# Optimization experiments

Measured on AMD Instinct MI355X. Metric: run time of the kernel, lower is better.

Reference implementation:

```python
import jax, jax.numpy as jnp
import numpy as np

# ---- static configuration (matches init_kwargs / input_specs) ----
B, T, C = 32, 4096, 3
SCALES = 128
KLF = 10                      # kernel_length_factor
OUT_H, OUT_W = 224, 224
PRECISION = 12
N_PSI = 2 ** PRECISION        # 4096 samples of the integrated wavelet
XMIN, XMAX = -8.0, 8.0        # pywt 'mexh' support
SPAN = XMAX - XMIN
STEP = SPAN / (N_PSI - 1)     # x_master[1] - x_master[0]
MAX_SCALE = T // (2 * KLF)
SCALES_VEC = np.logspace(np.log10(2.0), np.log10(MAX_SCALE), SCALES).astype(np.float32)

# Per-scale gather indices (static: derived from constant scales_vec / x_master grid)
# j = floor(arange(scale*span + 1) / (scale*step)), clipped to valid range.
J_LIST = []
for s in SCALES_VEC:
    s = float(s)
    n = int(np.ceil(s * SPAN + 1.0))
    j = np.floor(np.arange(n, dtype=np.float64) / (s * STEP)).astype(np.int32)
    J_LIST.append(np.clip(j, 0, N_PSI - 1))


def _mexh_int_psi():
    """Integrated Mexican-hat wavelet, exactly as pywt wavefun + CWTLayer build()."""
    x = np.linspace(XMIN, XMAX, N_PSI)
    psi = (2.0 / (np.sqrt(3.0) * np.pi ** 0.25)) * (1.0 - x ** 2) * np.exp(-x ** 2 / 2.0)
    dt = x[1] - x[0]
    int_psi = np.cumsum(psi) * dt
    int_psi -= np.mean(int_psi)
    int_psi /= np.sqrt(np.sum(np.abs(int_psi) ** 2))
    return int_psi.astype(np.float32)


def setup_inputs() -> dict:
    key = jax.random.key(0)
    x = jax.random.normal(key, (B, T, C), dtype=jnp.float32)
    int_psi_base = jnp.asarray(_mexh_int_psi())
    return {"x": x, "int_psi_base": int_psi_base}


def reference(x, int_psi_base):
    pad = min((N_PSI - 1) // 2, T - 1)                       # 2047
    xp = jnp.pad(x, ((0, 0), (pad, pad), (0, 0)), mode="reflect")
    xp = jnp.transpose(xp, (2, 0, 1)).reshape(C * B, T + 2 * pad, 1)  # NWC

    coefs = []
    for s, j in zip(SCALES_VEC, J_LIST):
        # dynamic-length wavelet kernel built by gather, flipped (as in the layer)
        kern = jnp.flip(jnp.take(int_psi_base, jnp.asarray(j), axis=0))[:, None, None]  # (K,1,1) WIO
        conv = jax.lax.conv_general_dilated(
            xp, kern, window_strides=(1,), padding="VALID",
            dimension_numbers=("NWC", "WIO", "NWC"))[..., 0]  # (CB, Lc)
        coef = -jnp.sqrt(jnp.float32(s)) * (conv[:, 1:] - conv[:, :-1])
        d = max((coef.shape[-1] - T) // 2, 0)
        coefs.append(jax.lax.dynamic_slice_in_dim(coef, d, T, axis=1))

    out = jnp.stack(coefs, axis=1)                    # (C*B, SCALES, T)
    out = out.reshape(C, B, SCALES, T).transpose(1, 2, 3, 0)  # (B, SCALES, T, C)
    out = jax.image.resize(out, (B, OUT_H, OUT_W, C), method="bilinear")
    return out
```

## Files before the change

### kernel.cpp

```cpp
#include <hip/hip_runtime.h>
#include <cmath>
#include <cstdint>


constexpr int C_TP     = 8190;
constexpr int C_XROWS  = 8192;
constexpr long long C_HSTRIDE = 3776;
constexpr int C_HGUARD = 160;
constexpr int C_NCLS   = 9;
constexpr int C_RW     = 8;
constexpr int C_NCH    = 28;
constexpr int C_NW     = 224;
constexpr int C_SIGP   = 128;
constexpr int C_M      = 512;
constexpr int C_NP     = 7;
constexpr int C_SQ     = 64;

typedef float v2f __attribute__((ext_vector_type(2)));
typedef float v4f __attribute__((ext_vector_type(4)));

__device__ __forceinline__ void scale_params(int i, float& s32, int& K, int& d, double& a) {
  const double l2   = log10(2.0);
  const double l204 = log10(204.0);
  double step = (l204 - l2) / 127.0;
  double e = (i == 127) ? l204 : ((double)i * step + l2);
  double sv = pow(10.0, e);
  s32 = (float)sv;
  double sp = (double)s32;
  K = (int)ceil(sp * 16.0 + 1.0);
  d = (4094 - K) >> 1;
  a = sp * (16.0 / 4095.0);
}

__global__ __launch_bounds__(256) void k_build_H(const float* __restrict__ int_psi,
                                                 const float* __restrict__ x,
                                                 float* __restrict__ Hbuf,
                                                 int* __restrict__ meta,
                                                 float* __restrict__ xpQ,
                                                 float* __restrict__ OT) {
  int i   = blockIdx.x;
  int cls = blockIdx.y;

  if (cls == 9) {
    float4* otz = (float4*)OT + (long long)i * 7168;
    float4 z4 = make_float4(0.f, 0.f, 0.f, 0.f);
    for (int q = threadIdx.x; q < 7168; q += 256) otz[q] = z4;
    for (int q = threadIdx.x; q < 8192; q += 256) {
      int idx = i * 8192 + q;
      int r   = idx & 127;
      int p   = idx >> 7;
      int g   = r >> 2;
      int e   = r & 3;
      float val = 0.f;
      if (e < 3 && p < C_TP) {
        int t = p - 2047;
        if (t < 0) t = -t;
        else if (t > 4095) t = 8190 - t;
        val = x[(g * 4096 + t) * 3 + e];
      }
      xpQ[idx] = val;
    }
    return;
  }

  float s32; int K, d; double a;
  scale_params(i, s32, K, d, a);

  int wr = (cls < 7) ? ((cls == 0) ? 7 : cls) : ((cls == 7) ? 0 : 223);
  double ks = 4096.0 / 224.0;
  double sf = ((double)wr + 0.5) * ks - 0.5;
  int t_lo = (int)floor(sf - ks) + 1;
  int t_hi = (int)ceil(sf + ks) - 1;
  if (t_lo < 0) t_lo = 0;
  if (t_hi > 4095) t_hi = 4095;
  int nt  = t_hi - t_lo + 1;
  int npv = nt + 1;

  int p_lo = t_lo + d;
  int Lh   = K + npv - 1;
  int kr   = (cls == 0) ? 1 : ((cls == 8) ? 31 : 0);
  int off0 = p_lo - 128 * kr;
  int shift = off0 & 3;
  int offA  = off0 - shift;
  int rowLen = (shift + Lh + 3) & ~3;

  __shared__ double Wt_sh[40];
  __shared__ float  v_shf[40];
  __shared__ float  kern_sh[3352];

  float* rowFull = Hbuf + (long long)(i * C_NCLS + cls) * C_HSTRIDE;
  int g0 = C_HGUARD + shift;
  int g1 = g0 + Lh;
  for (int q = threadIdx.x; q < g0; q += 256) rowFull[q] = 0.f;
  for (int q = g1 + threadIdx.x; q < (int)C_HSTRIDE; q += 256) rowFull[q] = 0.f;

  if (threadIdx.x == 0) {
    double Z = 0.0;
    for (int t = 0; t < nt; ++t) {
      double wv = 1.0 - fabs(sf - (double)(t + t_lo)) / ks;
      if (wv < 0.0) wv = 0.0;
      Wt_sh[t] = wv; Z += wv;
    }
    for (int t = 0; t < nt; ++t) Wt_sh[t] = Wt_sh[t] / Z;
    double sq = sqrt((double)s32);
    for (int q = 0; q < 40; ++q) {
      double wm1 = (q >= 1 && q <= nt)  ? Wt_sh[q - 1] : 0.0;
      double w0  = (q < nt)             ? Wt_sh[q]     : 0.0;
      v_shf[q] = (float)(-sq * (wm1 - w0));
    }
  }

  float* kernp = kern_sh + 40;
  int fillN = K + 80;
  for (int q = threadIdx.x; q < fillN; q += 256) {
    int tau = q - 40;
    float kv = 0.f;
    if (tau >= 0 && tau < K) {
      int u = K - 1 - tau;
      int jj = (int)floor((double)u / a);
      jj = jj < 0 ? 0 : (jj > 4095 ? 4095 : jj);
      kv = int_psi[jj];
    }
    kern_sh[q] = kv;
  }
  __syncthreads();

  float* row = rowFull + C_HGUARD;
  for (int q = threadIdx.x; q < Lh; q += 256) {
    float acc = 0.f;
    for (int t = 0; t < npv; ++t) acc += v_shf[t] * kernp[q - t];
    row[shift + q] = acc;
  }
  if (threadIdx.x == 0) {
    meta[(i * C_NCLS + cls) * 2 + 0] = offA;
    meta[(i * C_NCLS + cls) * 2 + 1] = rowLen;
  }
}

__global__ __launch_bounds__(64, 4) void k_cwt_main(const float* __restrict__ xpQ,
                                                    const float* __restrict__ Hbuf,
                                                    const int* __restrict__ meta,
                                                    float* __restrict__ OT) {
  int piece = blockIdx.x;
  int chunk = blockIdx.y;
  int i     = 127 - blockIdx.z;
  int lane  = threadIdx.x;
  int g     = lane & 31;
  int half  = lane >> 5;

  __shared__ v4f Hs[C_RW][C_SQ];

  v2f accL[C_RW], accH[C_RW];
  const float* rowP[C_RW];
  int startj[C_RW];
  int U0 = 0x7fffffff, U1 = 0;
#pragma unroll
  for (int j = 0; j < C_RW; ++j) {
    accL[j] = (v2f){0.f, 0.f};
    accH[j] = (v2f){0.f, 0.f};
    int w = chunk * C_RW + j;
    int cls = (w == 0) ? 7 : ((w == 223) ? 8 : (w % 7));
    int k = w / 7;
    int base = i * C_NCLS + cls;
    int offA = meta[base * 2 + 0];
    int rl   = meta[base * 2 + 1];
    int start = offA + 128 * k;
    startj[j] = start;
    if (start < U0) U0 = start;
    if (start + rl > U1) U1 = start + rl;
    rowP[j] = Hbuf + (long long)base * C_HSTRIDE;
  }

  int m0 = U0 + piece * C_M;
  int m1 = m0 + C_M; if (m1 > U1) m1 = U1;
  if (m0 >= m1) return;

  int len = m1 - m0;
  int nIt = (len + 7) >> 3;

  for (int ph = 0; ph < 2; ++ph) {
    int it0 = ph << 5;
    if (it0 >= nIt) break;
    int it1 = nIt < it0 + 32 ? nIt : it0 + 32;
    int qn  = 2 * (it1 - it0);

#pragma unroll
    for (int j = 0; j < C_RW; ++j) {
      const float* src = rowP[j] + (C_HGUARD + m0 - startj[j]) + 8 * it0;
      if (lane < qn) Hs[j][lane] = *(const v4f*)(src + 4 * lane);
    }
    __syncthreads();

    const float* xr = xpQ + ((long long)(m0 + 8 * it0 + 4 * half) << 7) + (g << 2);
#pragma unroll 2
    for (int it = it0; it < it1; ++it) {
      v4f xv0 = *(const v4f*)(xr);
      v4f xv1 = *(const v4f*)(xr + 128);
      v4f xv2 = *(const v4f*)(xr + 256);
      v4f xv3 = *(const v4f*)(xr + 384);
      xr += 1024;
      int lq = 2 * (it - it0) + half;
#pragma unroll
      for (int j = 0; j < C_RW; ++j) {
        v4f h = Hs[j][lq];
        accL[j] += xv0.xy * h.x; accH[j] += xv0.zw * h.x;
        accL[j] += xv1.xy * h.y; accH[j] += xv1.zw * h.y;
        accL[j] += xv2.xy * h.z; accH[j] += xv2.zw * h.z;
        accL[j] += xv3.xy * h.w; accH[j] += xv3.zw * h.w;
      }
    }
    __syncthreads();
  }

#pragma unroll
  for (int j = 0; j < C_RW; ++j) {
    float s0 = accL[j].x, s1 = accL[j].y, s2 = accH[j].x, s3 = accH[j].y;
    s0 += __shfl_xor(s0, 32);
    s1 += __shfl_xor(s1, 32);
    s2 += __shfl_xor(s2, 32);
    s3 += __shfl_xor(s3, 32);
    if (lane < 32) {
      int w = chunk * C_RW + j;
      float* dst = OT + ((long long)i * C_NW + w) * C_SIGP;
      atomicAdd(dst + g,      s0);
      atomicAdd(dst + 32 + g, s1);
      atomicAdd(dst + 64 + g, s2);
      atomicAdd(dst + 96 + g, s3);
    }
  }
}

__global__ __launch_bounds__(256) void k_final(const float* __restrict__ OT,
                                               float* __restrict__ out) {
  int wt = blockIdx.x;
  int h  = blockIdx.y;

  float inv = 128.0f / 224.0f;
  float sg = ((float)h + 0.5f) * inv - 0.5f;
  float sgf = floorf(sg);
  int s0 = (int)sgf;
  float fr = sg - sgf;
  int r0, r1;
  if (s0 < 0)        { r0 = 0;   r1 = 0;   fr = 0.f; }
  else if (s0 >= 127){ r0 = 127; r1 = 127; fr = 0.f; }
  else               { r0 = s0;  r1 = s0 + 1; }

  __shared__ float sh0[8 * 132];
  __shared__ float sh1[8 * 132];
  for (int q = threadIdx.x; q < 1024; q += 256) {
    int wp  = q >> 7;
    int sg2 = q & 127;
    int wg  = wt * 8 + wp;
    sh0[wp * 132 + sg2] = OT[((long long)r0 * C_NW + wg) * C_SIGP + sg2];
    sh1[wp * 132 + sg2] = OT[((long long)r1 * C_NW + wg) * C_SIGP + sg2];
  }
  __syncthreads();

  int b  = threadIdx.x >> 3;
  int wp = threadIdx.x & 7;
  int obase = ((b * 224 + h) * 224 + wt * 8 + wp) * 3;
#pragma unroll
  for (int c = 0; c < 3; ++c) {
    int sidx = wp * 132 + c * 32 + b;
    float a0 = sh0[sidx];
    float a1 = sh1[sidx];
    out[obase + c] = (1.0f - fr) * a0 + fr * a1;
  }
}

extern "C" void kernel_launch(void* const* d_in, const int* in_sizes, int n_in,
                              void* d_out, int out_size, void* d_ws, size_t ws_size,
                              hipStream_t stream) {
  const float* x       = (const float*)d_in[0];
  const float* int_psi = (const float*)d_in[1];
  float* out = (float*)d_out;

  float* xpQ  = (float*)d_ws;
  float* Hbuf = xpQ + (long long)C_XROWS * C_SIGP;
  int*   meta = (int*)(Hbuf + (long long)128 * C_NCLS * C_HSTRIDE);
  float* OT   = (float*)(meta + 2304);

  k_build_H<<<dim3(128, 10), dim3(256), 0, stream>>>(int_psi, x, Hbuf, meta, xpQ, OT);
  k_cwt_main<<<dim3(C_NP, C_NCH, 128), dim3(64), 0, stream>>>(xpQ, Hbuf, meta, OT);
  k_final<<<dim3(28, 224), dim3(256), 0, stream>>>(OT, out);
}
```

Before: 204.1 us.

## Widen CWT register tile to 16 output columns and prefetch signal rows

Each CWT block now accumulates 16 output columns instead of 8, so every loaded signal vector is reused across twice as many filter rows. The number of column chunks is halved and the shared filter staging is split into four 16-iteration phases with 32-entry buffers. The signal loads are software-pipelined one iteration ahead. Filter row pointers are recomputed during staging instead of held in registers, and the H buffer gets a zeroed front pad and a larger stride to cover out-of-range reads. The wider tile doubles accumulator registers, which may lower occupancy, and the prefetch reads one row group past the end.

Result: slower. 412.2 us (+102.0%).

```diff
diff --git a/kernel.cpp b/kernel.cpp
--- a/kernel.cpp
+++ b/kernel.cpp
@@ -5,16 +5,17 @@
 
 constexpr int C_TP     = 8190;
 constexpr int C_XROWS  = 8192;
-constexpr long long C_HSTRIDE = 3776;
+constexpr long long C_HSTRIDE = 3968;
 constexpr int C_HGUARD = 160;
+constexpr int C_HPAD   = 512;
 constexpr int C_NCLS   = 9;
-constexpr int C_RW     = 8;
-constexpr int C_NCH    = 28;
+constexpr int C_RW     = 16;
+constexpr int C_NCH    = 14;
 constexpr int C_NW     = 224;
 constexpr int C_SIGP   = 128;
 constexpr int C_M      = 512;
-constexpr int C_NP     = 7;
-constexpr int C_SQ     = 64;
+constexpr int C_NP     = 8;
+constexpr int C_SQ     = 32;
 
 typedef float v2f __attribute__((ext_vector_type(2)));
 typedef float v4f __attribute__((ext_vector_type(4)));
@@ -45,6 +46,10 @@
     float4* otz = (float4*)OT + (long long)i * 7168;
     float4 z4 = make_float4(0.f, 0.f, 0.f, 0.f);
     for (int q = threadIdx.x; q < 7168; q += 256) otz[q] = z4;
+    if (i == 0) {
+      float* pad = Hbuf - C_HPAD;
+      for (int q = threadIdx.x; q < C_HPAD; q += 256) pad[q] = 0.f;
+    }
     for (int q = threadIdx.x; q < 8192; q += 256) {
       int idx = i * 8192 + q;
       int r   = idx & 127;
@@ -151,8 +156,6 @@
   __shared__ v4f Hs[C_RW][C_SQ];
 
   v2f accL[C_RW], accH[C_RW];
-  const float* rowP[C_RW];
-  int startj[C_RW];
   int U0 = 0x7fffffff, U1 = 0;
 #pragma unroll
   for (int j = 0; j < C_RW; ++j) {
@@ -160,54 +163,67 @@
     accH[j] = (v2f){0.f, 0.f};
     int w = chunk * C_RW + j;
     int cls = (w == 0) ? 7 : ((w == 223) ? 8 : (w % 7));
-    int k = w / 7;
     int base = i * C_NCLS + cls;
     int offA = meta[base * 2 + 0];
     int rl   = meta[base * 2 + 1];
-    int start = offA + 128 * k;
-    startj[j] = start;
+    int start = offA + 128 * (w / 7);
     if (start < U0) U0 = start;
     if (start + rl > U1) U1 = start + rl;
-    rowP[j] = Hbuf + (long long)base * C_HSTRIDE;
   }
 
   int m0 = U0 + piece * C_M;
   int m1 = m0 + C_M; if (m1 > U1) m1 = U1;
   if (m0 >= m1) return;
 
-  int len = m1 - m0;
-  int nIt = (len + 7) >> 3;
-
-  for (int ph = 0; ph < 2; ++ph) {
-    int it0 = ph << 5;
+  int nIt = (m1 - m0 + 7) >> 3;
+
+  for (int ph = 0; ph < 4; ++ph) {
+    int it0 = ph << 4;
     if (it0 >= nIt) break;
-    int it1 = nIt < it0 + 32 ? nIt : it0 + 32;
+    int it1 = nIt < it0 + 16 ? nIt : it0 + 16;
     int qn  = 2 * (it1 - it0);
 
-#pragma unroll
-    for (int j = 0; j < C_RW; ++j) {
-      const float* src = rowP[j] + (C_HGUARD + m0 - startj[j]) + 8 * it0;
-      if (lane < qn) Hs[j][lane] = *(const v4f*)(src + 4 * lane);
+    {
+      int ln = lane & 31;
+      if (ln < qn) {
+#pragma unroll
+        for (int jj = 0; jj < C_RW; jj += 2) {
+          int j = jj + half;
+          int w = chunk * C_RW + j;
+          int cls = (w == 0) ? 7 : ((w == 223) ? 8 : (w % 7));
+          int base = i * C_NCLS + cls;
+          int start = meta[base * 2 + 0] + 128 * (w / 7);
+          const float* src = Hbuf + (long long)base * C_HSTRIDE
+                           + (C_HGUARD + m0 - start) + 8 * it0;
+          Hs[j][ln] = *(const v4f*)(src + 4 * ln);
+        }
+      }
     }
     __syncthreads();
 
     const float* xr = xpQ + ((long long)(m0 + 8 * it0 + 4 * half) << 7) + (g << 2);
+    v4f c0 = *(const v4f*)(xr);
+    v4f c1 = *(const v4f*)(xr + 128);
+    v4f c2 = *(const v4f*)(xr + 256);
+    v4f c3 = *(const v4f*)(xr + 384);
+    xr += 1024;
 #pragma unroll 2
     for (int it = it0; it < it1; ++it) {
-      v4f xv0 = *(const v4f*)(xr);
-      v4f xv1 = *(const v4f*)(xr + 128);
-      v4f xv2 = *(const v4f*)(xr + 256);
-      v4f xv3 = *(const v4f*)(xr + 384);
+      v4f n0 = *(const v4f*)(xr);
+      v4f n1 = *(const v4f*)(xr + 128);
+      v4f n2 = *(const v4f*)(xr + 256);
+      v4f n3 = *(const v4f*)(xr + 384);
       xr += 1024;
       int lq = 2 * (it - it0) + half;
 #pragma unroll
       for (int j = 0; j < C_RW; ++j) {
         v4f h = Hs[j][lq];
-        accL[j] += xv0.xy * h.x; accH[j] += xv0.zw * h.x;
-        accL[j] += xv1.xy * h.y; accH[j] += xv1.zw * h.y;
-        accL[j] += xv2.xy * h.z; accH[j] += xv2.zw * h.z;
-        accL[j] += xv3.xy * h.w; accH[j] += xv3.zw * h.w;
+        accL[j] += c0.xy * h.x; accH[j] += c0.zw * h.x;
+        accL[j] += c1.xy * h.y; accH[j] += c1.zw * h.y;
+        accL[j] += c2.xy * h.z; accH[j] += c2.zw * h.z;
+        accL[j] += c3.xy * h.w; accH[j] += c3.zw * h.w;
       }
+      c0 = n0; c1 = n1; c2 = n2; c3 = n3;
     }
     __syncthreads();
   }
@@ -276,7 +292,7 @@
   float* out = (float*)d_out;
 
   float* xpQ  = (float*)d_ws;
-  float* Hbuf = xpQ + (long long)C_XROWS * C_SIGP;
+  float* Hbuf = xpQ + (long long)C_XROWS * C_SIGP + C_HPAD;
   int*   meta = (int*)(Hbuf + (long long)128 * C_NCLS * C_HSTRIDE);
   float* OT   = (float*)(meta + 2304);
 
```

## Drop LDS staging in CWT main kernel; split iterations across two waves

Applied to the files above, without the earlier changes.

The main convolution kernel no longer stages wavelet rows in shared memory and no longer uses barriers. It reads the wavelet coefficients directly from global memory as wave-uniform vector loads and software-prefetches the next signal rows into registers. The block grows to two waves, each handling half of the time-step iterations, with its own atomic accumulation. Each lane now covers two adjacent signal columns, which removes the cross-half shuffle reduction. In exchange it doubles the atomics per output and relies on caches to serve the repeated global reads of the wavelet rows.

New measurement: 395.4 us. +93.7%, slower.

```diff
diff --git a/kernel.cpp b/kernel.cpp
--- a/kernel.cpp
+++ b/kernel.cpp
@@ -14,7 +14,6 @@
 constexpr int C_SIGP   = 128;
 constexpr int C_M      = 512;
 constexpr int C_NP     = 7;
-constexpr int C_SQ     = 64;
 
 typedef float v2f __attribute__((ext_vector_type(2)));
 typedef float v4f __attribute__((ext_vector_type(4)));
@@ -137,97 +136,120 @@
   }
 }
 
-__global__ __launch_bounds__(64, 4) void k_cwt_main(const float* __restrict__ xpQ,
-                                                    const float* __restrict__ Hbuf,
-                                                    const int* __restrict__ meta,
-                                                    float* __restrict__ OT) {
+
+#define JSET(J) \
+  const int wJ##J   = chunk * C_RW + J; \
+  const int cls##J  = (wJ##J == 0) ? 7 : ((wJ##J == 223) ? 8 : (wJ##J % 7)); \
+  const int base##J = i * C_NCLS + cls##J; \
+  const int start##J = meta[base##J * 2 + 0] + 128 * (wJ##J / 7); \
+  const int end##J   = start##J + meta[base##J * 2 + 1];
+
+#define JPTR(J) \
+  const float* hp##J = Hbuf + (long long)base##J * C_HSTRIDE + (C_HGUARD + m0 - start##J);
+
+__global__ __launch_bounds__(128, 4) void k_cwt_main(const float* __restrict__ xpQ,
+                                                     const float* __restrict__ Hbuf,
+                                                     const int* __restrict__ meta,
+                                                     float* __restrict__ OT) {
   int piece = blockIdx.x;
   int chunk = blockIdx.y;
   int i     = 127 - blockIdx.z;
-  int lane  = threadIdx.x;
-  int g     = lane & 31;
-  int half  = lane >> 5;
-
-  __shared__ v4f Hs[C_RW][C_SQ];
-
-  v2f accL[C_RW], accH[C_RW];
-  const float* rowP[C_RW];
-  int startj[C_RW];
-  int U0 = 0x7fffffff, U1 = 0;
-#pragma unroll
-  for (int j = 0; j < C_RW; ++j) {
-    accL[j] = (v2f){0.f, 0.f};
-    accH[j] = (v2f){0.f, 0.f};
-    int w = chunk * C_RW + j;
-    int cls = (w == 0) ? 7 : ((w == 223) ? 8 : (w % 7));
-    int k = w / 7;
-    int base = i * C_NCLS + cls;
-    int offA = meta[base * 2 + 0];
-    int rl   = meta[base * 2 + 1];
-    int start = offA + 128 * k;
-    startj[j] = start;
-    if (start < U0) U0 = start;
-    if (start + rl > U1) U1 = start + rl;
-    rowP[j] = Hbuf + (long long)base * C_HSTRIDE;
-  }
+  int tid   = threadIdx.x;
+  int lane  = tid & 63;
+  int wid   = tid >> 6;
+
+  JSET(0) JSET(1) JSET(2) JSET(3) JSET(4) JSET(5) JSET(6) JSET(7)
+
+  int U0 = start0;
+  U0 = start1 < U0 ? start1 : U0;  U0 = start2 < U0 ? start2 : U0;
+  U0 = start3 < U0 ? start3 : U0;  U0 = start4 < U0 ? start4 : U0;
+  U0 = start5 < U0 ? start5 : U0;  U0 = start6 < U0 ? start6 : U0;
+  U0 = start7 < U0 ? start7 : U0;
+  int U1 = end0;
+  U1 = end1 > U1 ? end1 : U1;  U1 = end2 > U1 ? end2 : U1;
+  U1 = end3 > U1 ? end3 : U1;  U1 = end4 > U1 ? end4 : U1;
+  U1 = end5 > U1 ? end5 : U1;  U1 = end6 > U1 ? end6 : U1;
+  U1 = end7 > U1 ? end7 : U1;
 
   int m0 = U0 + piece * C_M;
   int m1 = m0 + C_M; if (m1 > U1) m1 = U1;
   if (m0 >= m1) return;
 
-  int len = m1 - m0;
-  int nIt = (len + 7) >> 3;
-
-  for (int ph = 0; ph < 2; ++ph) {
-    int it0 = ph << 5;
-    if (it0 >= nIt) break;
-    int it1 = nIt < it0 + 32 ? nIt : it0 + 32;
-    int qn  = 2 * (it1 - it0);
-
-#pragma unroll
-    for (int j = 0; j < C_RW; ++j) {
-      const float* src = rowP[j] + (C_HGUARD + m0 - startj[j]) + 8 * it0;
-      if (lane < qn) Hs[j][lane] = *(const v4f*)(src + 4 * lane);
-    }
-    __syncthreads();
-
-    const float* xr = xpQ + ((long long)(m0 + 8 * it0 + 4 * half) << 7) + (g << 2);
+  int nIt  = (m1 - m0 + 7) >> 3;
+  int nItW = (nIt + 1) >> 1;
+  int itLo = wid ? nItW : 0;
+  int itHi = wid ? nIt  : nItW;
+  if (itLo >= itHi) return;
+
+  JPTR(0) JPTR(1) JPTR(2) JPTR(3) JPTR(4) JPTR(5) JPTR(6) JPTR(7)
+
+  v2f acc0 = (v2f){0.f,0.f}, acc1 = (v2f){0.f,0.f}, acc2 = (v2f){0.f,0.f},
+      acc3 = (v2f){0.f,0.f}, acc4 = (v2f){0.f,0.f}, acc5 = (v2f){0.f,0.f},
+      acc6 = (v2f){0.f,0.f}, acc7 = (v2f){0.f,0.f};
+
+  const float* xr = xpQ + ((long long)(m0 + 8 * itLo) << 7) + (lane << 1);
+  v2f c0 = *(const v2f*)(xr +   0);
+  v2f c1 = *(const v2f*)(xr + 128);
+  v2f c2 = *(const v2f*)(xr + 256);
+  v2f c3 = *(const v2f*)(xr + 384);
+  v2f c4 = *(const v2f*)(xr + 512);
+  v2f c5 = *(const v2f*)(xr + 640);
+  v2f c6 = *(const v2f*)(xr + 768);
+  v2f c7 = *(const v2f*)(xr + 896);
+  xr += 1024;
+
+  v4f hA0 = *(const v4f*)(hp0 + 8 * itLo);
+  v4f hA1 = *(const v4f*)(hp1 + 8 * itLo);
+  v4f hA2 = *(const v4f*)(hp2 + 8 * itLo);
+  v4f hA3 = *(const v4f*)(hp3 + 8 * itLo);
+  v4f hA4 = *(const v4f*)(hp4 + 8 * itLo);
+  v4f hA5 = *(const v4f*)(hp5 + 8 * itLo);
+  v4f hA6 = *(const v4f*)(hp6 + 8 * itLo);
+  v4f hA7 = *(const v4f*)(hp7 + 8 * itLo);
+
+#define LOADN \
+  v2f n0 = *(const v2f*)(xr +   0); v2f n1 = *(const v2f*)(xr + 128); \
+  v2f n2 = *(const v2f*)(xr + 256); v2f n3 = *(const v2f*)(xr + 384); \
+  v2f n4 = *(const v2f*)(xr + 512); v2f n5 = *(const v2f*)(xr + 640); \
+  v2f n6 = *(const v2f*)(xr + 768); v2f n7 = *(const v2f*)(xr + 896); \
+  xr += 1024;
+#define LOADHB(J) v4f hB##J = *(const v4f*)(hp##J + 8 * it + 4);
+#define LOADHA(J) hA##J = *(const v4f*)(hp##J + 8 * it + 8);
+#define FMAA(J) acc##J += c0 * hA##J.x; acc##J += c1 * hA##J.y; \
+                acc##J += c2 * hA##J.z; acc##J += c3 * hA##J.w;
+#define FMAB(J) acc##J += c4 * hB##J.x; acc##J += c5 * hB##J.y; \
+                acc##J += c6 * hB##J.z; acc##J += c7 * hB##J.w;
+
 #pragma unroll 2
-    for (int it = it0; it < it1; ++it) {
-      v4f xv0 = *(const v4f*)(xr);
-      v4f xv1 = *(const v4f*)(xr + 128);
-      v4f xv2 = *(const v4f*)(xr + 256);
-      v4f xv3 = *(const v4f*)(xr + 384);
-      xr += 1024;
-      int lq = 2 * (it - it0) + half;
-#pragma unroll
-      for (int j = 0; j < C_RW; ++j) {
-        v4f h = Hs[j][lq];
-        accL[j] += xv0.xy * h.x; accH[j] += xv0.zw * h.x;
-        accL[j] += xv1.xy * h.y; accH[j] += xv1.zw * h.y;
-        accL[j] += xv2.xy * h.z; accH[j] += xv2.zw * h.z;
-        accL[j] += xv3.xy * h.w; accH[j] += xv3.zw * h.w;
-      }
-    }
-    __syncthreads();
-  }
-
-#pragma unroll
-  for (int j = 0; j < C_RW; ++j) {
-    float s0 = accL[j].x, s1 = accL[j].y, s2 = accH[j].x, s3 = accH[j].y;
-    s0 += __shfl_xor(s0, 32);
-    s1 += __shfl_xor(s1, 32);
-    s2 += __shfl_xor(s2, 32);
-    s3 += __shfl_xor(s3, 32);
-    if (lane < 32) {
-      int w = chunk * C_RW + j;
-      float* dst = OT + ((long long)i * C_NW + w) * C_SIGP;
-      atomicAdd(dst + g,      s0);
-      atomicAdd(dst + 32 + g, s1);
-      atomicAdd(dst + 64 + g, s2);
-      atomicAdd(dst + 96 + g, s3);
-    }
-  }
+  for (int it = itLo; it < itHi; ++it) {
+    LOADN
+    LOADHB(0) LOADHB(1) LOADHB(2) LOADHB(3)
+    LOADHB(4) LOADHB(5) LOADHB(6) LOADHB(7)
+    FMAA(0) FMAA(1) FMAA(2) FMAA(3)
+    FMAA(4) FMAA(5) FMAA(6) FMAA(7)
+    LOADHA(0) LOADHA(1) LOADHA(2) LOADHA(3)
+    LOADHA(4) LOADHA(5) LOADHA(6) LOADHA(7)
+    FMAB(0) FMAB(1) FMAB(2) FMAB(3)
+    FMAB(4) FMAB(5) FMAB(6) FMAB(7)
+    c0 = n0; c1 = n1; c2 = n2; c3 = n3;
+    c4 = n4; c5 = n5; c6 = n6; c7 = n7;
+  }
+
+  int g2 = lane >> 1;
+  int s0 = ((lane & 1) << 6) + g2;
+#define JATOM(J) { \
+    float* dst = OT + ((long long)i * C_NW + wJ##J) * C_SIGP; \
+    atomicAdd(dst + s0,      acc##J.x); \
+    atomicAdd(dst + s0 + 32, acc##J.y); }
+  JATOM(0) JATOM(1) JATOM(2) JATOM(3) JATOM(4) JATOM(5) JATOM(6) JATOM(7)
+#undef JSET
+#undef JPTR
+#undef LOADN
+#undef LOADHB
+#undef LOADHA
+#undef FMAA
+#undef FMAB
+#undef JATOM
 }
 
 __global__ __launch_bounds__(256) void k_final(const float* __restrict__ OT,
@@ -281,6 +303,6 @@
   float* OT   = (float*)(meta + 2304);
 
   k_build_H<<<dim3(128, 10), dim3(256), 0, stream>>>(int_psi, x, Hbuf, meta, xpQ, OT);
-  k_cwt_main<<<dim3(C_NP, C_NCH, 128), dim3(64), 0, stream>>>(xpQ, Hbuf, meta, OT);
+  k_cwt_main<<<dim3(C_NP, C_NCH, 128), dim3(128), 0, stream>>>(xpQ, Hbuf, meta, OT);
   k_final<<<dim3(28, 224), dim3(256), 0, stream>>>(OT, out);
 }
```
